# Kernel optimization log

Measured on AMD Instinct MI355X. Metric: run time of the kernel, lower is better.

## Reference

```python
import math
import jax, jax.numpy as jnp
import numpy as np

MUL = 16          # multiplicity of 0e and 1o in irreps_in/out
DIM = 4 * MUL     # 16 scalars + 16 vectors*3 = 64 channels
DIAMETER = 5.0
STEPS = (1.0, 1.0, 1.0)
NB = 8            # num_radial_basis


def gen_lattice():
    r = DIAMETER / 2
    ax = [jnp.arange(-math.floor(r / s), math.floor(r / s) + 1.0) * s for s in STEPS]
    return jnp.stack(jnp.meshgrid(*ax, indexing='ij'), axis=-1)  # [kx,ky,kz,3]


def radial_emb(r):
    # soft_one_hot_linspace(basis='smooth_finite', cutoff=True)
    values = jnp.linspace(0.0, DIAMETER / 2, NB + 2)[1:-1]
    step = (DIAMETER / 2) / (NB + 1)
    diff = (r[..., None] - values) / step
    den = jnp.maximum(1.0 - diff * diff, 1e-9)  # avoid nan grads outside support
    return jnp.where(jnp.abs(diff) < 1.0, 1.14136 * jnp.exp(2.0 - 1.0 / den), 0.0)


def sph_l01(vec):
    # spherical harmonics l=0,1 with normalize=True, normalization='component'
    n = jnp.linalg.norm(vec, axis=-1, keepdims=True)
    unit = jnp.where(n > 0, vec / jnp.where(n > 0, n, 1.0), 0.0)
    y0 = jnp.ones(vec.shape[:-1] + (1,), vec.dtype)
    return jnp.concatenate([y0, math.sqrt(3.0) * unit], axis=-1)  # [...,4]


def tp_right(w, sh):
    # Right operand of fully-connected tensor product (in x sh -> out):
    # returns per-lattice-point matrix R [L, DIM_in, DIM_out] s.t. TP(x, sh) = x @ R.
    # Paths (uvw): 0e*0e->0e, 0e*1o->1o, 1o*0e->1o, 1o*1o->0e.
    L = w.shape[0]
    W = w.reshape(L, 4, MUL, MUL)      # per-path weights [u, w] (mul_sh = 1)
    y0, y1 = sh[:, 0], sh[:, 1:4]
    a = 1.0 / math.sqrt(2.0 * MUL)     # fan-in: mul_in * mul_sh * 2 paths per output
    eye3 = jnp.eye(3, dtype=w.dtype)
    Rss = a * W[:, 0] * y0[:, None, None]                                            # [L,16,16]
    Rsv = a * jnp.einsum('luw,lm->luwm', W[:, 1], y1).reshape(L, MUL, 3 * MUL)        # CG = identity
    Rvv = a * jnp.einsum('luw,l,mn->lumwn', W[:, 2], y0, eye3).reshape(L, 3 * MUL, 3 * MUL)
    Rvs = (a / math.sqrt(3.0)) * jnp.einsum('luw,lm->lumw', W[:, 3], y1).reshape(L, 3 * MUL, MUL)  # CG = delta/sqrt3
    return jnp.concatenate([jnp.concatenate([Rss, Rsv], -1),
                            jnp.concatenate([Rvs, Rvv], -1)], 1)  # [L,64,64]


def reference(x, linear_weight, weight):
    lattice = gen_lattice()
    emb = radial_emb(jnp.linalg.norm(lattice, axis=-1))   # [kx,ky,kz,NB]
    sh = sph_l01(lattice)                                  # [kx,ky,kz,4]
    # self-connection: irrep-wise Linear with 1/sqrt(fan_in)
    Wl = linear_weight.reshape(2, MUL, MUL) / math.sqrt(MUL)
    xs = x[..., :MUL]
    xv = x[..., MUL:].reshape(x.shape[:-1] + (MUL, 3))
    sc = jnp.concatenate([
        jnp.einsum('...u,uw->...w', xs, Wl[0]),
        jnp.einsum('...um,uw->...wm', xv, Wl[1]).reshape(x.shape[:-1] + (3 * MUL,))], -1)
    # radial-MLP weights -> per-voxel TP kernel
    kx, ky, kz = sh.shape[:3]
    w = (emb.reshape(-1, NB) @ weight) / (kx * ky * kz)    # [L, 4*MUL*MUL]
    k = tp_right(w, sh.reshape(-1, 4)).reshape(kx, ky, kz, DIM, DIM)
    y = jax.lax.conv_general_dilated(x, k, (1, 1, 1), 'SAME',
                                     dimension_numbers=('NXYZC', 'XYZIO', 'NXYZC'))
    return sc + y


def setup_inputs():
    key = jax.random.key(0)
    k1, k2, k3 = jax.random.split(key, 3)
    return {
        'x': jax.random.normal(k1, (2, 40, 40, 40, DIM), jnp.float32),
        'linear_weight': jax.random.normal(k2, (2 * MUL * MUL,), jnp.float32),
        'weight': jax.random.normal(k3, (NB, 4 * MUL * MUL), jnp.float32),
    }
```

## Files before the change

kernel.cpp:

```cpp
#include <hip/hip_runtime.h>
#include <hip/hip_bf16.h>


typedef __bf16 bf16x8 __attribute__((ext_vector_type(8)));
typedef float f32x4 __attribute__((ext_vector_type(4)));

#define XP_BYTES 21807104
#define COLSTRIDE 6160
#define LDS_BYTES 49280

__global__ __launch_bounds__(256) void prep(const float* __restrict__ x,
                                            const float* __restrict__ lw,
                                            const float* __restrict__ wt,
                                            ushort* __restrict__ xp,
                                            ushort* __restrict__ Kb) {
  if (blockIdx.x < 5324) {
    int tid = blockIdx.x * 256 + threadIdx.x;
    int c8 = (tid & 7) * 8;
    int v = tid >> 3;
    int zi = v % 44; int t = v / 44;
    int yi = t % 44; t /= 44;
    int xi = t % 44; int n = t / 44;
    int4 st;
    if (xi >= 2 && xi < 42 && yi >= 2 && yi < 42 && zi >= 2 && zi < 42) {
      const float* src = x + ((((size_t)n * 40 + (xi - 2)) * 40 + (yi - 2)) * 40 + (zi - 2)) * 64 + c8;
      float4 f0 = ((const float4*)src)[0];
      float4 f1 = ((const float4*)src)[1];
      union { __hip_bfloat16 h[8]; int4 v4; } u;
      u.h[0] = __float2bfloat16(f0.x); u.h[1] = __float2bfloat16(f0.y);
      u.h[2] = __float2bfloat16(f0.z); u.h[3] = __float2bfloat16(f0.w);
      u.h[4] = __float2bfloat16(f1.x); u.h[5] = __float2bfloat16(f1.y);
      u.h[6] = __float2bfloat16(f1.z); u.h[7] = __float2bfloat16(f1.w);
      st = u.v4;
    } else {
      st = make_int4(0, 0, 0, 0);
    }
    ((int4*)xp)[tid] = st;
  } else {
    int tid = (blockIdx.x - 5324) * 256 + threadIdx.x;
    int j  = tid & 7;
    int o  = (tid >> 3) & 63;
    int kg = (tid >> 9) & 7;
    int l  = tid >> 12;
    int i  = kg * 8 + j;

    int ix = l / 25; int rem = l - ix * 25; int iy = rem / 5; int iz = rem - iy * 5;
    float cx = (float)(ix - 2), cy = (float)(iy - 2), cz = (float)(iz - 2);
    float r = sqrtf(cx * cx + cy * cy + cz * cz);

    float e[8];
    const float step = 2.5f / 9.0f;
    #pragma unroll
    for (int b = 0; b < 8; b++) {
      float diff = (r - (float)(b + 1) * step) / step;
      float den = fmaxf(1.0f - diff * diff, 1e-9f);
      e[b] = (fabsf(diff) < 1.0f) ? 1.14136f * expf(2.0f - 1.0f / den) : 0.0f;
    }
    float inv = (r > 0.0f) ? 1.0f / r : 0.0f;
    const float s3 = 1.7320508075688772f;
    float y1[3] = { s3 * cx * inv, s3 * cy * inv, s3 * cz * inv };
    const float a  = 0.17677669529663687f;
    const float a3 = 0.10206207261596575f;

    auto wElem = [&](int c, int u, int w) -> float {
      const float* p = wt + c * 256 + u * 16 + w;
      float s = 0.f;
      #pragma unroll
      for (int b = 0; b < 8; b++) s += e[b] * p[b * 1024];
      return s * (1.0f / 125.0f);
    };

    float val;
    if (i < 16) {
      if (o < 16) {
        val = a * wElem(0, i, o);
      } else {
        int om = o - 16; int w = om / 3, m = om - 3 * w;
        val = a * wElem(1, i, w) * y1[m];
      }
    } else {
      int im = i - 16; int u = im / 3, m = im - 3 * u;
      if (o < 16) {
        val = a3 * wElem(3, u, o) * y1[m];
      } else {
        int om = o - 16; int w = om / 3, nn = om - 3 * w;
        val = (m == nn) ? a * wElem(2, u, w) : 0.0f;
      }
    }
    if (l == 62) {
      if (i < 16 && o < 16) {
        val += lw[i * 16 + o] * 0.25f;
      } else if (i >= 16 && o >= 16) {
        int im = i - 16, om = o - 16;
        int u = im / 3, m = im - 3 * u;
        int w = om / 3, nn = om - 3 * w;
        if (m == nn) val += lw[256 + u * 16 + w] * 0.25f;
      }
    }
    __hip_bfloat16 h = __float2bfloat16(val);
    Kb[tid] = *(ushort*)&h;
  }
}

__global__ __launch_bounds__(256, 3) void conv_mfma(const ushort* __restrict__ xp_,
                                                    const ushort* __restrict__ Kb_,
                                                    float* __restrict__ out) {
  const char* xpB = (const char*)xp_;
  const char* KbB = (const char*)Kb_;
  __shared__ __align__(16) char smem[LDS_BYTES];

  const int tid = threadIdx.x;
  const int lane = tid & 63;
  const int wv = tid >> 6;
  const int wm = wv & 1, wn = wv >> 1;
  const int g = lane >> 4, ol = lane & 15;

  int bid = blockIdx.x;
  int yg = bid % 10; int t = bid / 10;
  int xx = t % 40; int n = t / 40;
  int y0 = yg * 4;
  int p0 = ((n * 40 + xx) * 40 + y0) * 40;

  int lanebase[5];
  #pragma unroll
  for (int mt = 0; mt < 5; mt++) {
    int r = wm * 80 + mt * 16 + ol;
    int yrel = r / 40, z = r - yrel * 40;
    lanebase[mt] = g * COLSTRIDE + (yrel * 44 + z) * 16;
  }

  const int bbase = g * 1024 + wn * 512 + ol * 16;

  f32x4 acc[5][2] = {};

  const size_t slab0 = ((((size_t)n * 44 + xx) * 44 + y0) * 44) * 128;

  for (int dx = 0; dx < 5; dx++) {
    const char* slab = xpB + slab0 + (size_t)dx * (44 * 44 * 128);
    int4 v[6];
    #pragma unroll
    for (int it = 0; it < 6; it++)
      v[it] = *(const int4*)(slab + ((size_t)(it * 256 + tid)) * 16);
    if (dx > 0) __syncthreads();
    #pragma unroll
    for (int it = 0; it < 6; it++) {
      int c = it * 256 + tid;
      *(int4*)(smem + (c & 7) * COLSTRIDE + (c >> 3) * 16) = v[it];
    }
    #pragma unroll
    for (int it = 0; it < 5; it++)
      v[it] = *(const int4*)(slab + ((size_t)((it + 6) * 256 + tid)) * 16);
    #pragma unroll
    for (int it = 0; it < 5; it++) {
      int c = (it + 6) * 256 + tid;
      *(int4*)(smem + (c & 7) * COLSTRIDE + (c >> 3) * 16) = v[it];
    }
    __syncthreads();

    const char* kbdx = KbB + (size_t)dx * 25 * 8192 + bbase;
    #pragma unroll
    for (int dy = 0; dy < 5; dy++) {
      #pragma unroll
      for (int dz = 0; dz < 5; dz++) {
        const int toff = (dy * 44 + dz) * 16;
        bf16x8 a[5][2], b[2][2];
        #pragma unroll
        for (int mt = 0; mt < 5; mt++)
          #pragma unroll
          for (int kc = 0; kc < 2; kc++)
            a[mt][kc] = *(const bf16x8*)(smem + lanebase[mt] + kc * (4 * COLSTRIDE) + toff);
        const char* kb = kbdx + (dy * 5 + dz) * 8192;
        #pragma unroll
        for (int kc = 0; kc < 2; kc++)
          #pragma unroll
          for (int nt = 0; nt < 2; nt++)
            b[kc][nt] = *(const bf16x8*)(kb + kc * 4096 + nt * 256);
        #pragma unroll
        for (int kc = 0; kc < 2; kc++)
          #pragma unroll
          for (int nt = 0; nt < 2; nt++)
            #pragma unroll
            for (int mt = 0; mt < 5; mt++)
              acc[mt][nt] = __builtin_amdgcn_mfma_f32_16x16x32_bf16(a[mt][kc], b[kc][nt], acc[mt][nt], 0, 0, 0);
      }
    }
  }

  #pragma unroll
  for (int mt = 0; mt < 5; mt++)
    #pragma unroll
    for (int nt = 0; nt < 2; nt++)
      #pragma unroll
      for (int j = 0; j < 4; j++) {
        int p = p0 + wm * 80 + mt * 16 + g * 4 + j;
        out[(size_t)p * 64 + wn * 32 + nt * 16 + ol] = acc[mt][nt][j];
      }
}

extern "C" void kernel_launch(void* const* d_in, const int* in_sizes, int n_in,
                              void* d_out, int out_size, void* d_ws, size_t ws_size,
                              hipStream_t stream) {
  const float* x  = (const float*)d_in[0];
  const float* lw = (const float*)d_in[1];
  const float* wt = (const float*)d_in[2];
  float* out = (float*)d_out;
  ushort* xp = (ushort*)d_ws;
  ushort* Kb = (ushort*)((char*)d_ws + XP_BYTES);

  prep<<<7324, 256, 0, stream>>>(x, lw, wt, xp, Kb);
  conv_mfma<<<800, 256, 0, stream>>>(xp, Kb, out);
}
```

Baseline: 256.5 us.

## Fuse input padding and bf16 conversion into conv, enlarge tiles, coalesce output

Drops the separate padded bf16 copy of the input. The conv kernel now reads fp32 x directly, converts it to bf16 and zero-fills the halo while staging each x-plane into LDS, and skips out-of-range dx planes. Each block now covers 8 y-rows and all 64 output channels (400 blocks, occupancy hint 2), so every wave handles 80 rows by 4 N-tiles. The epilogue goes through LDS so it can issue coalesced 16-byte stores. This removes a large workspace write and read, but only 400 blocks remain, the staging loop is longer, and register pressure is higher.

```diff
diff --git a/kernel.cpp b/kernel.cpp
--- a/kernel.cpp
+++ b/kernel.cpp
@@ -5,180 +5,162 @@
 typedef __bf16 bf16x8 __attribute__((ext_vector_type(8)));
 typedef float f32x4 __attribute__((ext_vector_type(4)));
 
-#define XP_BYTES 21807104
-#define COLSTRIDE 6160
-#define LDS_BYTES 49280
-
-__global__ __launch_bounds__(256) void prep(const float* __restrict__ x,
-                                            const float* __restrict__ lw,
-                                            const float* __restrict__ wt,
-                                            ushort* __restrict__ xp,
-                                            ushort* __restrict__ Kb) {
-  if (blockIdx.x < 5324) {
-    int tid = blockIdx.x * 256 + threadIdx.x;
-    int c8 = (tid & 7) * 8;
-    int v = tid >> 3;
-    int zi = v % 44; int t = v / 44;
-    int yi = t % 44; t /= 44;
-    int xi = t % 44; int n = t / 44;
-    int4 st;
-    if (xi >= 2 && xi < 42 && yi >= 2 && yi < 42 && zi >= 2 && zi < 42) {
-      const float* src = x + ((((size_t)n * 40 + (xi - 2)) * 40 + (yi - 2)) * 40 + (zi - 2)) * 64 + c8;
-      float4 f0 = ((const float4*)src)[0];
-      float4 f1 = ((const float4*)src)[1];
-      union { __hip_bfloat16 h[8]; int4 v4; } u;
-      u.h[0] = __float2bfloat16(f0.x); u.h[1] = __float2bfloat16(f0.y);
-      u.h[2] = __float2bfloat16(f0.z); u.h[3] = __float2bfloat16(f0.w);
-      u.h[4] = __float2bfloat16(f1.x); u.h[5] = __float2bfloat16(f1.y);
-      u.h[6] = __float2bfloat16(f1.z); u.h[7] = __float2bfloat16(f1.w);
-      st = u.v4;
+#define COLCH 577
+#define COLSTRIDE (COLCH * 16)
+#define LDS_BYTES (8 * COLSTRIDE)
+
+__global__ __launch_bounds__(256) void build_k(const float* __restrict__ lw,
+                                               const float* __restrict__ wt,
+                                               ushort* __restrict__ Kb) {
+  int tid = blockIdx.x * 256 + threadIdx.x;
+  int j  = tid & 7;
+  int o  = (tid >> 3) & 63;
+  int kg = (tid >> 9) & 7;
+  int l  = tid >> 12;
+  int i  = kg * 8 + j;
+
+  int ix = l / 25; int rem = l - ix * 25; int iy = rem / 5; int iz = rem - iy * 5;
+  float cx = (float)(ix - 2), cy = (float)(iy - 2), cz = (float)(iz - 2);
+  float r = sqrtf(cx * cx + cy * cy + cz * cz);
+
+  float e[8];
+  const float step = 2.5f / 9.0f;
+  #pragma unroll
+  for (int b = 0; b < 8; b++) {
+    float diff = (r - (float)(b + 1) * step) / step;
+    float den = fmaxf(1.0f - diff * diff, 1e-9f);
+    e[b] = (fabsf(diff) < 1.0f) ? 1.14136f * expf(2.0f - 1.0f / den) : 0.0f;
+  }
+  float inv = (r > 0.0f) ? 1.0f / r : 0.0f;
+  const float s3 = 1.7320508075688772f;
+  float y1[3] = { s3 * cx * inv, s3 * cy * inv, s3 * cz * inv };
+  const float a  = 0.17677669529663687f;
+  const float a3 = 0.10206207261596575f;
+
+  auto wElem = [&](int c, int u, int w) -> float {
+    const float* p = wt + c * 256 + u * 16 + w;
+    float s = 0.f;
+    #pragma unroll
+    for (int b = 0; b < 8; b++) s += e[b] * p[b * 1024];
+    return s * (1.0f / 125.0f);
+  };
+
+  float val;
+  if (i < 16) {
+    if (o < 16) {
+      val = a * wElem(0, i, o);
     } else {
-      st = make_int4(0, 0, 0, 0);
-    }
-    ((int4*)xp)[tid] = st;
+      int om = o - 16; int w = om / 3, m = om - 3 * w;
+      val = a * wElem(1, i, w) * y1[m];
+    }
   } else {
-    int tid = (blockIdx.x - 5324) * 256 + threadIdx.x;
-    int j  = tid & 7;
-    int o  = (tid >> 3) & 63;
-    int kg = (tid >> 9) & 7;
-    int l  = tid >> 12;
-    int i  = kg * 8 + j;
-
-    int ix = l / 25; int rem = l - ix * 25; int iy = rem / 5; int iz = rem - iy * 5;
-    float cx = (float)(ix - 2), cy = (float)(iy - 2), cz = (float)(iz - 2);
-    float r = sqrtf(cx * cx + cy * cy + cz * cz);
-
-    float e[8];
-    const float step = 2.5f / 9.0f;
-    #pragma unroll
-    for (int b = 0; b < 8; b++) {
-      float diff = (r - (float)(b + 1) * step) / step;
-      float den = fmaxf(1.0f - diff * diff, 1e-9f);
-      e[b] = (fabsf(diff) < 1.0f) ? 1.14136f * expf(2.0f - 1.0f / den) : 0.0f;
-    }
-    float inv = (r > 0.0f) ? 1.0f / r : 0.0f;
-    const float s3 = 1.7320508075688772f;
-    float y1[3] = { s3 * cx * inv, s3 * cy * inv, s3 * cz * inv };
-    const float a  = 0.17677669529663687f;
-    const float a3 = 0.10206207261596575f;
-
-    auto wElem = [&](int c, int u, int w) -> float {
-      const float* p = wt + c * 256 + u * 16 + w;
-      float s = 0.f;
-      #pragma unroll
-      for (int b = 0; b < 8; b++) s += e[b] * p[b * 1024];
-      return s * (1.0f / 125.0f);
-    };
-
-    float val;
-    if (i < 16) {
-      if (o < 16) {
-        val = a * wElem(0, i, o);
-      } else {
-        int om = o - 16; int w = om / 3, m = om - 3 * w;
-        val = a * wElem(1, i, w) * y1[m];
-      }
+    int im = i - 16; int u = im / 3, m = im - 3 * u;
+    if (o < 16) {
+      val = a3 * wElem(3, u, o) * y1[m];
     } else {
-      int im = i - 16; int u = im / 3, m = im - 3 * u;
-      if (o < 16) {
-        val = a3 * wElem(3, u, o) * y1[m];
-      } else {
-        int om = o - 16; int w = om / 3, nn = om - 3 * w;
-        val = (m == nn) ? a * wElem(2, u, w) : 0.0f;
-      }
-    }
-    if (l == 62) {
-      if (i < 16 && o < 16) {
-        val += lw[i * 16 + o] * 0.25f;
-      } else if (i >= 16 && o >= 16) {
-        int im = i - 16, om = o - 16;
-        int u = im / 3, m = im - 3 * u;
-        int w = om / 3, nn = om - 3 * w;
-        if (m == nn) val += lw[256 + u * 16 + w] * 0.25f;
-      }
-    }
-    __hip_bfloat16 h = __float2bfloat16(val);
-    Kb[tid] = *(ushort*)&h;
-  }
+      int om = o - 16; int w = om / 3, nn = om - 3 * w;
+      val = (m == nn) ? a * wElem(2, u, w) : 0.0f;
+    }
+  }
+  if (l == 62) {
+    if (i < 16 && o < 16) {
+      val += lw[i * 16 + o] * 0.25f;
+    } else if (i >= 16 && o >= 16) {
+      int im = i - 16, om = o - 16;
+      int u = im / 3, m = im - 3 * u;
+      int w = om / 3, nn = om - 3 * w;
+      if (m == nn) val += lw[256 + u * 16 + w] * 0.25f;
+    }
+  }
+  __hip_bfloat16 h = __float2bfloat16(val);
+  Kb[tid] = *(ushort*)&h;
 }
 
-__global__ __launch_bounds__(256, 3) void conv_mfma(const ushort* __restrict__ xp_,
+__global__ __launch_bounds__(256, 2) void conv_mfma(const float* __restrict__ x,
                                                     const ushort* __restrict__ Kb_,
                                                     float* __restrict__ out) {
-  const char* xpB = (const char*)xp_;
   const char* KbB = (const char*)Kb_;
   __shared__ __align__(16) char smem[LDS_BYTES];
 
   const int tid = threadIdx.x;
   const int lane = tid & 63;
   const int wv = tid >> 6;
-  const int wm = wv & 1, wn = wv >> 1;
   const int g = lane >> 4, ol = lane & 15;
 
   int bid = blockIdx.x;
-  int yg = bid % 10; int t = bid / 10;
-  int xx = t % 40; int n = t / 40;
-  int y0 = yg * 4;
-  int p0 = ((n * 40 + xx) * 40 + y0) * 40;
+  int yg = bid % 5; int t = bid / 5;
+  int ox = t % 40; int n = t / 40;
+  int y0 = yg * 8;
+  int p0 = ((n * 40 + ox) * 40 + y0) * 40;
 
   int lanebase[5];
   #pragma unroll
   for (int mt = 0; mt < 5; mt++) {
-    int r = wm * 80 + mt * 16 + ol;
-    int yrel = r / 40, z = r - yrel * 40;
-    lanebase[mt] = g * COLSTRIDE + (yrel * 44 + z) * 16;
-  }
-
-  const int bbase = g * 1024 + wn * 512 + ol * 16;
-
-  f32x4 acc[5][2] = {};
-
-  const size_t slab0 = ((((size_t)n * 44 + xx) * 44 + y0) * 44) * 128;
+    int r = wv * 80 + mt * 16 + ol;
+    int oyr = r / 40, oz = r - oyr * 40;
+    lanebase[mt] = g * COLSTRIDE + (oyr * 48 + oz) * 16;
+  }
+  const int bbase = g * 1024 + ol * 16;
+
+  f32x4 acc[5][4] = {};
+
+  const float* xn = x + (size_t)n * 40 * 40 * 40 * 64;
 
   for (int dx = 0; dx < 5; dx++) {
-    const char* slab = xpB + slab0 + (size_t)dx * (44 * 44 * 128);
-    int4 v[6];
-    #pragma unroll
-    for (int it = 0; it < 6; it++)
-      v[it] = *(const int4*)(slab + ((size_t)(it * 256 + tid)) * 16);
-    if (dx > 0) __syncthreads();
-    #pragma unroll
-    for (int it = 0; it < 6; it++) {
+    int ix = ox + dx - 2;
+    if (ix < 0 || ix >= 40) continue;
+    __syncthreads();
+    const float* xpl = xn + (size_t)ix * 40 * 40 * 64;
+    for (int it = 0; it < 17; it++) {
       int c = it * 256 + tid;
-      *(int4*)(smem + (c & 7) * COLSTRIDE + (c >> 3) * 16) = v[it];
-    }
-    #pragma unroll
-    for (int it = 0; it < 5; it++)
-      v[it] = *(const int4*)(slab + ((size_t)((it + 6) * 256 + tid)) * 16);
-    #pragma unroll
-    for (int it = 0; it < 5; it++) {
-      int c = (it + 6) * 256 + tid;
-      *(int4*)(smem + (c & 7) * COLSTRIDE + (c >> 3) * 16) = v[it];
+      if (c < 4224) {
+        int ch8 = c & 7;
+        int rowsrc = c >> 3;
+        int yrel = rowsrc / 44;
+        int zr = rowsrc - yrel * 44;
+        int iy = y0 - 2 + yrel;
+        int iz = zr - 2;
+        int4 st = make_int4(0, 0, 0, 0);
+        if (iy >= 0 && iy < 40 && iz >= 0 && iz < 40) {
+          const float* src = xpl + ((size_t)iy * 40 + iz) * 64 + ch8 * 8;
+          float4 f0 = ((const float4*)src)[0];
+          float4 f1 = ((const float4*)src)[1];
+          union { __hip_bfloat16 h[8]; int4 v4; } u;
+          u.h[0] = __float2bfloat16(f0.x); u.h[1] = __float2bfloat16(f0.y);
+          u.h[2] = __float2bfloat16(f0.z); u.h[3] = __float2bfloat16(f0.w);
+          u.h[4] = __float2bfloat16(f1.x); u.h[5] = __float2bfloat16(f1.y);
+          u.h[6] = __float2bfloat16(f1.z); u.h[7] = __float2bfloat16(f1.w);
+          st = u.v4;
+        }
+        *(int4*)(smem + ch8 * COLSTRIDE + (yrel * 48 + zr) * 16) = st;
+      }
     }
     __syncthreads();
 
     const char* kbdx = KbB + (size_t)dx * 25 * 8192 + bbase;
-    #pragma unroll
+    #pragma unroll 1
     for (int dy = 0; dy < 5; dy++) {
+      const int dyoff = dy * 48 * 16;
+      const char* kbdy = kbdx + dy * 5 * 8192;
       #pragma unroll
       for (int dz = 0; dz < 5; dz++) {
-        const int toff = (dy * 44 + dz) * 16;
-        bf16x8 a[5][2], b[2][2];
+        const int toff = dyoff + dz * 16;
+        bf16x8 a[5][2], b[2][4];
         #pragma unroll
         for (int mt = 0; mt < 5; mt++)
           #pragma unroll
           for (int kc = 0; kc < 2; kc++)
             a[mt][kc] = *(const bf16x8*)(smem + lanebase[mt] + kc * (4 * COLSTRIDE) + toff);
-        const char* kb = kbdx + (dy * 5 + dz) * 8192;
+        const char* kb = kbdy + dz * 8192;
         #pragma unroll
         for (int kc = 0; kc < 2; kc++)
           #pragma unroll
-          for (int nt = 0; nt < 2; nt++)
+          for (int nt = 0; nt < 4; nt++)
             b[kc][nt] = *(const bf16x8*)(kb + kc * 4096 + nt * 256);
         #pragma unroll
         for (int kc = 0; kc < 2; kc++)
           #pragma unroll
-          for (int nt = 0; nt < 2; nt++)
+          for (int nt = 0; nt < 4; nt++)
             #pragma unroll
             for (int mt = 0; mt < 5; mt++)
               acc[mt][nt] = __builtin_amdgcn_mfma_f32_16x16x32_bf16(a[mt][kc], b[kc][nt], acc[mt][nt], 0, 0, 0);
@@ -186,15 +168,22 @@
     }
   }
 
-  #pragma unroll
-  for (int mt = 0; mt < 5; mt++)
+  __syncthreads();
+  float* sw = (float*)(smem + wv * (16 * 66 * 4));
+  #pragma unroll 1
+  for (int mt = 0; mt < 5; mt++) {
     #pragma unroll
-    for (int nt = 0; nt < 2; nt++)
+    for (int nt = 0; nt < 4; nt++)
       #pragma unroll
-      for (int j = 0; j < 4; j++) {
-        int p = p0 + wm * 80 + mt * 16 + g * 4 + j;
-        out[(size_t)p * 64 + wn * 32 + nt * 16 + ol] = acc[mt][nt][j];
-      }
+      for (int j = 0; j < 4; j++)
+        sw[(g * 4 + j) * 66 + nt * 16 + ol] = acc[mt][nt][j];
+    float* outb = out + (size_t)(p0 + wv * 80 + mt * 16) * 64;
+    #pragma unroll
+    for (int i = 0; i < 4; i++) {
+      int4 vv = *(int4*)&sw[(i * 4 + g) * 66 + ol * 4];
+      ((int4*)outb)[i * 64 + lane] = vv;
+    }
+  }
 }
 
 extern "C" void kernel_launch(void* const* d_in, const int* in_sizes, int n_in,
@@ -204,9 +193,8 @@
   const float* lw = (const float*)d_in[1];
   const float* wt = (const float*)d_in[2];
   float* out = (float*)d_out;
-  ushort* xp = (ushort*)d_ws;
-  ushort* Kb = (ushort*)((char*)d_ws + XP_BYTES);
-
-  prep<<<7324, 256, 0, stream>>>(x, lw, wt, xp, Kb);
-  conv_mfma<<<800, 256, 0, stream>>>(xp, Kb, out);
+  ushort* Kb = (ushort*)d_ws;
+
+  build_k<<<2000, 256, 0, stream>>>(lw, wt, Kb);
+  conv_mfma<<<400, 256, 0, stream>>>(x, Kb, out);
 }
```

New measurement: 301.1 us. 1.17x slower.
